# Optimization experiments

Hardware: AMD Instinct MI355X
Metric: run time of the kernel (lower is better)

Reference implementation:

```python
import jax, jax.numpy as jnp
import numpy as np

N = 50000     # nodes
E = 800000    # edges (avg degree 16)
IN, HID, OUT = 128, 128, 64


def setup_inputs() -> dict:
    key = jax.random.key(0)
    ks = jax.random.split(key, 12)
    x = jax.random.normal(ks[0], (N, IN), jnp.float32)
    src = jax.random.randint(ks[1], (E,), 0, N)
    dst = jax.random.randint(ks[2], (E,), 0, N)

    def lin(k, i, o):
        return (jax.random.normal(k, (i, o), jnp.float32) / np.sqrt(i)).astype(jnp.float32)

    return {
        "x": x, "src": src, "dst": dst,
        "Ws0": lin(ks[3], IN, HID), "Wn0": lin(ks[4], IN, HID), "b0": jnp.zeros((HID,), jnp.float32),
        "Ws1": lin(ks[5], HID, HID), "Wn1": lin(ks[6], HID, HID), "b1": jnp.zeros((HID,), jnp.float32),
        "Ws2": lin(ks[7], HID, OUT), "Wn2": lin(ks[8], HID, OUT), "b2": jnp.zeros((OUT,), jnp.float32),
    }


def reference(x, src, dst, Ws0, Wn0, b0, Ws1, Wn1, b1, Ws2, Wn2, b2):
    # in-degree for mean aggregation (clamped to 1 like DGL's mean reducer on non-empty mailboxes)
    deg = jnp.maximum(
        jax.ops.segment_sum(jnp.ones((E,), jnp.float32), dst, num_segments=N), 1.0
    )[:, None]

    def sage_conv(h, Ws, Wn, b):
        # gather src features, sum-reduce onto dst, divide by degree -> mean aggregation
        agg = jax.ops.segment_sum(h[src], dst, num_segments=N)  # [N, d]
        mean = agg / deg
        return h @ Ws + mean @ Wn + b

    h = jax.nn.relu(sage_conv(x, Ws0, Wn0, b0))   # dropout in eval mode -> identity
    h = jax.nn.relu(sage_conv(h, Ws1, Wn1, b1))
    return sage_conv(h, Ws2, Wn2, b2)
```

## Files before the change

kernel.cpp:

```cpp
#include <hip/hip_runtime.h>

#define CAP    64
#define PASSES 4
#define CSTRIDE 16

typedef __attribute__((ext_vector_type(8))) short bf16x8;
typedef __attribute__((ext_vector_type(4))) float f32x4;

__device__ __forceinline__ unsigned short f2bf(float f) {
    unsigned u = __builtin_bit_cast(unsigned, f);
    u += 0x7fffu + ((u >> 16) & 1u);
    return (unsigned short)(u >> 16);
}
__device__ __forceinline__ float bf2f(unsigned short h) {
    unsigned u = ((unsigned)h) << 16;
    return __builtin_bit_cast(float, u);
}

__device__ __forceinline__ void gload_lds16(const void* g, void* lds) {
    __builtin_amdgcn_global_load_lds(
        (const __attribute__((address_space(1))) void*)g,
        (__attribute__((address_space(3))) void*)lds, 16, 0, 0);
}

__global__ __launch_bounds__(256)
void fill_bucket_kernel(const int* __restrict__ src, const int* __restrict__ dst,
                        int* __restrict__ cnt, unsigned short* __restrict__ slot,
                        int E, int nPerPass) {
    int t  = blockIdx.x * 256 + threadIdx.x;
    int e0 = t * 4;
    if (e0 >= E) return;
    int4 s4, d4;
    if (e0 + 4 <= E) {
        s4 = *reinterpret_cast<const int4*>(src + e0);
        d4 = *reinterpret_cast<const int4*>(dst + e0);
    } else {
        int r = E - e0;
        s4.x = src[e0];                  d4.x = dst[e0];
        s4.y = (r > 1) ? src[e0 + 1] : 0; d4.y = (r > 1) ? dst[e0 + 1] : -1;
        s4.z = (r > 2) ? src[e0 + 2] : 0; d4.z = (r > 2) ? dst[e0 + 2] : -1;
        s4.w = 0;                         d4.w = -1;
    }
    #pragma unroll
    for (int p = 0; p < PASSES; p++) {
        const int lo = p * nPerPass, hi = lo + nPerPass;
        if (d4.x >= lo && d4.x < hi) {
            int q = atomicAdd(&cnt[(size_t)d4.x * CSTRIDE], 1);
            if (q < CAP) slot[(size_t)d4.x * CAP + q] = (unsigned short)s4.x;
        }
        if (d4.y >= lo && d4.y < hi) {
            int q = atomicAdd(&cnt[(size_t)d4.y * CSTRIDE], 1);
            if (q < CAP) slot[(size_t)d4.y * CAP + q] = (unsigned short)s4.y;
        }
        if (d4.z >= lo && d4.z < hi) {
            int q = atomicAdd(&cnt[(size_t)d4.z * CSTRIDE], 1);
            if (q < CAP) slot[(size_t)d4.z * CAP + q] = (unsigned short)s4.z;
        }
        if (d4.w >= lo && d4.w < hi) {
            int q = atomicAdd(&cnt[(size_t)d4.w * CSTRIDE], 1);
            if (q < CAP) slot[(size_t)d4.w * CAP + q] = (unsigned short)s4.w;
        }
    }
}

__global__ __launch_bounds__(256)
void split_x_kernel(const float* __restrict__ x, unsigned short* __restrict__ xhi,
                    unsigned short* __restrict__ xlo, long long total4)
{
    long long i = (long long)blockIdx.x * 256 + threadIdx.x;
    if (i >= total4) return;
    float4 v = reinterpret_cast<const float4*>(x)[i];
    float f[4] = {v.x, v.y, v.z, v.w};
    unsigned short h4[4], l4[4];
    #pragma unroll
    for (int j = 0; j < 4; j++) {
        h4[j] = f2bf(f[j]);
        l4[j] = f2bf(f[j] - bf2f(h4[j]));
    }
    reinterpret_cast<ushort4*>(xhi)[i] = make_ushort4(h4[0], h4[1], h4[2], h4[3]);
    reinterpret_cast<ushort4*>(xlo)[i] = make_ushort4(l4[0], l4[1], l4[2], l4[3]);
}

__global__ __launch_bounds__(256)
void prep_w_all_kernel(const float* __restrict__ Ws0, const float* __restrict__ Wn0,
                       const float* __restrict__ Ws1, const float* __restrict__ Wn1,
                       const float* __restrict__ Ws2, const float* __restrict__ Wn2,
                       unsigned short* __restrict__ Wh0, unsigned short* __restrict__ Wl0,
                       unsigned short* __restrict__ Wh1, unsigned short* __restrict__ Wl1,
                       unsigned short* __restrict__ Wh2, unsigned short* __restrict__ Wl2)
{
    int b = blockIdx.x;
    const float *Ws, *Wn;
    unsigned short *Wthi, *Wtlo;
    int D, idx;
    if (b < 128)      { Ws = Ws0; Wn = Wn0; Wthi = Wh0; Wtlo = Wl0; D = 128; idx = b * 256 + threadIdx.x; }
    else if (b < 256) { Ws = Ws1; Wn = Wn1; Wthi = Wh1; Wtlo = Wl1; D = 128; idx = (b - 128) * 256 + threadIdx.x; }
    else              { Ws = Ws2; Wn = Wn2; Wthi = Wh2; Wtlo = Wl2; D = 64;  idx = (b - 256) * 256 + threadIdx.x; }
    int DT = 2 * D;
    if (idx >= 128 * DT) return;
    int k = idx / DT, col = idx % DT;
    float v = (col < D) ? Ws[k * D + col] : Wn[k * D + (col - D)];
    unsigned short hi = f2bf(v);
    unsigned short lo = f2bf(v - bf2f(hi));
    Wthi[col * 128 + k] = hi;
    Wtlo[col * 128 + k] = lo;
}

template<int DTOT>
__global__ __launch_bounds__(256)
void mfma_dual_kernel(const unsigned short* __restrict__ hhi, const unsigned short* __restrict__ hlo,
                      const unsigned short* __restrict__ Wthi, const unsigned short* __restrict__ Wtlo,
                      const float* __restrict__ bias,
                      float* __restrict__ hs, unsigned short* __restrict__ hn, int N)
{
    constexpr int D  = DTOT / 2;
    constexpr int NT = DTOT / 64;
    constexpr int MT = 4;

    __shared__ unsigned short Ahi_l[64 * 128];
    __shared__ unsigned short Alo_l[64 * 128];

    const int tid = threadIdx.x;
    const int wv  = tid >> 6;
    const int l   = tid & 63;
    const int lm  = l & 15;
    const int kg  = l >> 4;
    const int block0  = blockIdx.x * 64;
    const int colbase = wv * (NT * 16);

    {
        const int row_l = (l >> 4);
        const int col16 = l & 15;
        #pragma unroll
        for (int i = 0; i < 4; i++) {
            const int ldsoff = wv * 4096 + i * 1024;
            int row = wv * 16 + i * 4 + row_l;
            int k2  = ((col16 ^ (row & 15)) << 4);
            int rg  = block0 + row; if (rg > N - 1) rg = N - 1;
            gload_lds16((const char*)hhi + (size_t)rg * 256 + k2, (char*)Ahi_l + ldsoff);
            gload_lds16((const char*)hlo + (size_t)rg * 256 + k2, (char*)Alo_l + ldsoff);
        }
    }
    asm volatile("s_waitcnt vmcnt(0)" ::: "memory");
    __syncthreads();

    f32x4 acc[MT][NT];
    #pragma unroll
    for (int mt = 0; mt < MT; mt++)
        #pragma unroll
        for (int nt = 0; nt < NT; nt++)
            acc[mt][nt] = (f32x4){0.f, 0.f, 0.f, 0.f};

    const size_t bofs = (size_t)(colbase + lm) * 128 + kg * 8;

    #pragma unroll
    for (int c = 0; c < 4; c++) {
        bf16x8 bh[NT], bl[NT];
        #pragma unroll
        for (int nt = 0; nt < NT; nt++) {
            const size_t bo = bofs + (size_t)nt * 16 * 128 + c * 32;
            bh[nt] = *reinterpret_cast<const bf16x8*>(Wthi + bo);
            bl[nt] = *reinterpret_cast<const bf16x8*>(Wtlo + bo);
        }
        bf16x8 ah[MT], al[MT];
        #pragma unroll
        for (int mt = 0; mt < MT; mt++) {
            const int r   = mt * 16 + lm;
            const int off = r * 128 + (((kg + 4 * c) ^ lm) << 3);
            ah[mt] = *reinterpret_cast<const bf16x8*>(&Ahi_l[off]);
            al[mt] = *reinterpret_cast<const bf16x8*>(&Alo_l[off]);
        }
        #pragma unroll
        for (int nt = 0; nt < NT; nt++)
            #pragma unroll
            for (int mt = 0; mt < MT; mt++) {
                acc[mt][nt] = __builtin_amdgcn_mfma_f32_16x16x32_bf16(ah[mt], bh[nt], acc[mt][nt], 0, 0, 0);
                acc[mt][nt] = __builtin_amdgcn_mfma_f32_16x16x32_bf16(ah[mt], bl[nt], acc[mt][nt], 0, 0, 0);
                acc[mt][nt] = __builtin_amdgcn_mfma_f32_16x16x32_bf16(al[mt], bh[nt], acc[mt][nt], 0, 0, 0);
            }
    }

    #pragma unroll
    for (int nt = 0; nt < NT; nt++) {
        const int col = colbase + nt * 16 + lm;
        const float bb = (col < D) ? bias[col] : 0.f;
        #pragma unroll
        for (int mt = 0; mt < MT; mt++) {
            #pragma unroll
            for (int i = 0; i < 4; i++) {
                int n = block0 + mt * 16 + kg * 4 + i;
                if (n >= N) continue;
                float v = acc[mt][nt][i];
                if (col < D) hs[(size_t)n * D + col] = v + bb;
                else         hn[(size_t)n * D + (col - D)] = f2bf(v);
            }
        }
    }
}

template<int D, bool RELU, bool SPLIT>
__global__ __launch_bounds__(256)
void gather_finish_kernel(const unsigned short* __restrict__ hn, const float* __restrict__ hs,
                          const int* __restrict__ cnt, const unsigned short* __restrict__ slot,
                          unsigned short* __restrict__ ohi, unsigned short* __restrict__ olo,
                          float* __restrict__ ofp, int N)
{
    const int node = (int)(((size_t)blockIdx.x * blockDim.x + threadIdx.x) >> 6);
    const int lane = threadIdx.x & 63;
    if (node >= N) return;

    int deg = cnt[(size_t)node * CSTRIDE];
    if (deg > CAP) deg = CAP;

    const int si = (int)slot[(size_t)node * CAP + lane];

    float p0 = 0.f, p1 = 0.f, q0 = 0.f, q1 = 0.f;
    float r0a = 0.f, r1a = 0.f, t0 = 0.f, t1 = 0.f;

    for (int j = 0; j < deg; j += 8) {
        unsigned u[8];
        bool ok[8];
        #pragma unroll
        for (int k = 0; k < 8; k++) {
            int jj = j + k;
            int s = __shfl(si, jj, 64);
            if (s > N - 1) s = N - 1;
            if (s < 0) s = 0;
            ok[k] = jj < deg;
            if constexpr (D == 128)
                u[k] = *reinterpret_cast<const unsigned*>(&hn[(size_t)s * D + lane * 2]);
            else
                u[k] = (unsigned)hn[(size_t)s * D + lane];
        }
        #pragma unroll
        for (int k = 0; k < 8; k++) {
            float f0 = ok[k] ? bf2f((unsigned short)(u[k] & 0xffffu)) : 0.f;
            if constexpr (D == 128) {
                float f1 = ok[k] ? bf2f((unsigned short)(u[k] >> 16)) : 0.f;
                switch (k & 3) {
                    case 0: p0 += f0; p1 += f1; break;
                    case 1: q0 += f0; q1 += f1; break;
                    case 2: r0a += f0; r1a += f1; break;
                    default: t0 += f0; t1 += f1; break;
                }
            } else {
                switch (k & 3) {
                    case 0: p0 += f0; break;
                    case 1: q0 += f0; break;
                    case 2: r0a += f0; break;
                    default: t0 += f0; break;
                }
            }
        }
    }
    float acc0 = (p0 + q0) + (r0a + t0);
    float acc1 = (p1 + q1) + (r1a + t1);

    const float inv = 1.0f / (float)(deg > 1 ? deg : 1);

    if constexpr (D == 128) {
        float2 s2 = *reinterpret_cast<const float2*>(&hs[(size_t)node * D + lane * 2]);
        float v0 = fmaf(acc0, inv, s2.x);
        float v1 = fmaf(acc1, inv, s2.y);
        if (RELU) { v0 = fmaxf(v0, 0.f); v1 = fmaxf(v1, 0.f); }
        if constexpr (SPLIT) {
            unsigned short h0 = f2bf(v0), h1 = f2bf(v1);
            unsigned short l0 = f2bf(v0 - bf2f(h0)), l1 = f2bf(v1 - bf2f(h1));
            *reinterpret_cast<unsigned*>(&ohi[(size_t)node * D + lane * 2]) = (unsigned)h0 | ((unsigned)h1 << 16);
            *reinterpret_cast<unsigned*>(&olo[(size_t)node * D + lane * 2]) = (unsigned)l0 | ((unsigned)l1 << 16);
        } else {
            *reinterpret_cast<float2*>(&ofp[(size_t)node * D + lane * 2]) = make_float2(v0, v1);
        }
    } else {
        float s1 = hs[(size_t)node * D + lane];
        float v = fmaf(acc0, inv, s1);
        if (RELU) v = fmaxf(v, 0.f);
        if constexpr (SPLIT) {
            unsigned short h0 = f2bf(v);
            ohi[(size_t)node * D + lane] = h0;
            olo[(size_t)node * D + lane] = f2bf(v - bf2f(h0));
        } else {
            ofp[(size_t)node * D + lane] = v;
        }
    }
}

extern "C" void kernel_launch(void* const* d_in, const int* in_sizes, int n_in,
                              void* d_out, int out_size, void* d_ws, size_t ws_size,
                              hipStream_t stream)
{
    const float* x   = (const float*)d_in[0];
    const int*   src = (const int*)d_in[1];
    const int*   dst = (const int*)d_in[2];
    const float* Ws0 = (const float*)d_in[3];
    const float* Wn0 = (const float*)d_in[4];
    const float* b0  = (const float*)d_in[5];
    const float* Ws1 = (const float*)d_in[6];
    const float* Wn1 = (const float*)d_in[7];
    const float* b1  = (const float*)d_in[8];
    const float* Ws2 = (const float*)d_in[9];
    const float* Wn2 = (const float*)d_in[10];
    const float* b2  = (const float*)d_in[11];
    float* out = (float*)d_out;

    const int N = in_sizes[0] / 128;
    const int E = in_sizes[1];

    char* ws = (char*)d_ws;
    size_t off = 0;
    auto alloc = [&](size_t bytes) -> void* {
        void* p = ws + off;
        off += (bytes + 255) & ~(size_t)255;
        return p;
    };
    int*            cnt   = (int*)           alloc((size_t)N * CSTRIDE * 4);
    unsigned short* slot  = (unsigned short*)alloc((size_t)N * CAP * 2);
    unsigned short* xhi   = (unsigned short*)alloc((size_t)N * 128 * 2);
    unsigned short* xlo   = (unsigned short*)alloc((size_t)N * 128 * 2);
    float*          hsb   = (float*)         alloc((size_t)N * 128 * 4);
    unsigned short* hnb   = (unsigned short*)alloc((size_t)N * 128 * 2);
    unsigned short* Wh0   = (unsigned short*)alloc(256 * 128 * 2);
    unsigned short* Wl0   = (unsigned short*)alloc(256 * 128 * 2);
    unsigned short* Wh1   = (unsigned short*)alloc(256 * 128 * 2);
    unsigned short* Wl1   = (unsigned short*)alloc(256 * 128 * 2);
    unsigned short* Wh2   = (unsigned short*)alloc(128 * 128 * 2);
    unsigned short* Wl2   = (unsigned short*)alloc(128 * 128 * 2);

    hipMemsetAsync(cnt, 0, (size_t)N * CSTRIDE * 4, stream);
    const int nPerPass = (N + PASSES - 1) / PASSES;
    fill_bucket_kernel<<<(E / 4 + 255) / 256, 256, 0, stream>>>(src, dst, cnt, slot, E, nPerPass);

    long long total4 = (long long)N * 32;
    split_x_kernel<<<(int)((total4 + 255) / 256), 256, 0, stream>>>(x, xhi, xlo, total4);
    prep_w_all_kernel<<<320, 256, 0, stream>>>(Ws0, Wn0, Ws1, Wn1, Ws2, Wn2,
                                               Wh0, Wl0, Wh1, Wl1, Wh2, Wl2);

    const int rowTiles = (N + 63) / 64;
    const int gblocks  = (N + 3) / 4;

    mfma_dual_kernel<256><<<rowTiles, 256, 0, stream>>>(xhi, xlo, Wh0, Wl0, b0, hsb, hnb, N);
    gather_finish_kernel<128, true, true><<<gblocks, 256, 0, stream>>>(hnb, hsb, cnt, slot, xhi, xlo, nullptr, N);

    mfma_dual_kernel<256><<<rowTiles, 256, 0, stream>>>(xhi, xlo, Wh1, Wl1, b1, hsb, hnb, N);
    gather_finish_kernel<128, true, true><<<gblocks, 256, 0, stream>>>(hnb, hsb, cnt, slot, xhi, xlo, nullptr, N);

    mfma_dual_kernel<128><<<rowTiles, 256, 0, stream>>>(xhi, xlo, Wh2, Wl2, b2, hsb, hnb, N);
    gather_finish_kernel<64, false, false><<<gblocks, 256, 0, stream>>>(hnb, hsb, cnt, slot, nullptr, nullptr, out, N);
}
```

Measured before the change: 244.5 us.

## Replicate per-node edge buckets across block groups and compact to dense adjacency

Replaces the 4-pass atomic bucket fill with one pass that spreads each node's counter and slots over 8 replicas chosen by block index, which reduces atomic contention on hot counters. A new compaction kernel prefix-sums the replica counts per node and writes a dense 64-entry slot list plus a degree array for the gather kernels. This adds a kernel launch and extra memory traffic. It also caps each replica at 16 entries, so skewed degrees could drop edges that the old single 64-slot bucket kept.

```diff
diff --git a/kernel.cpp b/kernel.cpp
--- a/kernel.cpp
+++ b/kernel.cpp
@@ -1,8 +1,8 @@
 #include <hip/hip_runtime.h>
 
-#define CAP    64
-#define PASSES 4
-#define CSTRIDE 16
+#define CAP   64
+#define NREP  8
+#define CAPR  16
 
 typedef __attribute__((ext_vector_type(8))) short bf16x8;
 typedef __attribute__((ext_vector_type(4))) float f32x4;
@@ -25,42 +25,70 @@
 
 __global__ __launch_bounds__(256)
 void fill_bucket_kernel(const int* __restrict__ src, const int* __restrict__ dst,
-                        int* __restrict__ cnt, unsigned short* __restrict__ slot,
-                        int E, int nPerPass) {
+                        int* __restrict__ cnt8, unsigned short* __restrict__ slot8, int E) {
     int t  = blockIdx.x * 256 + threadIdx.x;
     int e0 = t * 4;
     if (e0 >= E) return;
+    const int r = blockIdx.x & (NREP - 1);
     int4 s4, d4;
     if (e0 + 4 <= E) {
         s4 = *reinterpret_cast<const int4*>(src + e0);
         d4 = *reinterpret_cast<const int4*>(dst + e0);
     } else {
-        int r = E - e0;
-        s4.x = src[e0];                  d4.x = dst[e0];
-        s4.y = (r > 1) ? src[e0 + 1] : 0; d4.y = (r > 1) ? dst[e0 + 1] : -1;
-        s4.z = (r > 2) ? src[e0 + 2] : 0; d4.z = (r > 2) ? dst[e0 + 2] : -1;
-        s4.w = 0;                         d4.w = -1;
-    }
-    #pragma unroll
-    for (int p = 0; p < PASSES; p++) {
-        const int lo = p * nPerPass, hi = lo + nPerPass;
-        if (d4.x >= lo && d4.x < hi) {
-            int q = atomicAdd(&cnt[(size_t)d4.x * CSTRIDE], 1);
-            if (q < CAP) slot[(size_t)d4.x * CAP + q] = (unsigned short)s4.x;
-        }
-        if (d4.y >= lo && d4.y < hi) {
-            int q = atomicAdd(&cnt[(size_t)d4.y * CSTRIDE], 1);
-            if (q < CAP) slot[(size_t)d4.y * CAP + q] = (unsigned short)s4.y;
-        }
-        if (d4.z >= lo && d4.z < hi) {
-            int q = atomicAdd(&cnt[(size_t)d4.z * CSTRIDE], 1);
-            if (q < CAP) slot[(size_t)d4.z * CAP + q] = (unsigned short)s4.z;
-        }
-        if (d4.w >= lo && d4.w < hi) {
-            int q = atomicAdd(&cnt[(size_t)d4.w * CSTRIDE], 1);
-            if (q < CAP) slot[(size_t)d4.w * CAP + q] = (unsigned short)s4.w;
-        }
-    }
+        int rr = E - e0;
+        s4.x = src[e0];                   d4.x = dst[e0];
+        s4.y = (rr > 1) ? src[e0 + 1] : 0; d4.y = (rr > 1) ? dst[e0 + 1] : -1;
+        s4.z = (rr > 2) ? src[e0 + 2] : 0; d4.z = (rr > 2) ? dst[e0 + 2] : -1;
+        s4.w = 0;                          d4.w = -1;
+    }
+    if (d4.x >= 0) {
+        int q = atomicAdd(&cnt8[(size_t)d4.x * NREP + r], 1);
+        if (q < CAPR) slot8[(size_t)d4.x * (NREP * CAPR) + r * CAPR + q] = (unsigned short)s4.x;
+    }
+    if (d4.y >= 0) {
+        int q = atomicAdd(&cnt8[(size_t)d4.y * NREP + r], 1);
+        if (q < CAPR) slot8[(size_t)d4.y * (NREP * CAPR) + r * CAPR + q] = (unsigned short)s4.y;
+    }
+    if (d4.z >= 0) {
+        int q = atomicAdd(&cnt8[(size_t)d4.z * NREP + r], 1);
+        if (q < CAPR) slot8[(size_t)d4.z * (NREP * CAPR) + r * CAPR + q] = (unsigned short)s4.z;
+    }
+    if (d4.w >= 0) {
+        int q = atomicAdd(&cnt8[(size_t)d4.w * NREP + r], 1);
+        if (q < CAPR) slot8[(size_t)d4.w * (NREP * CAPR) + r * CAPR + q] = (unsigned short)s4.w;
+    }
+}
+
+__global__ __launch_bounds__(256)
+void compact_kernel(const int* __restrict__ cnt8, const unsigned short* __restrict__ slot8,
+                    unsigned short* __restrict__ dense, int* __restrict__ deg, int N) {
+    const int node = (int)(((size_t)blockIdx.x * blockDim.x + threadIdx.x) >> 6);
+    const int l    = threadIdx.x & 63;
+    if (node >= N) return;
+
+    int cr = 0;
+    if (l < NREP) {
+        cr = cnt8[(size_t)node * NREP + l];
+        if (cr > CAPR) cr = CAPR;
+    }
+    int pre = cr;
+    #pragma unroll
+    for (int o = 1; o < NREP; o <<= 1) {
+        int v = __shfl_up(pre, o, 64);
+        if (l >= o) pre += v;
+    }
+    const int myr = l >> 3;
+    const int c   = __shfl(cr, myr, 64);
+    const int b   = __shfl(pre - cr, myr, 64);
+    int tot = __shfl(pre, NREP - 1, 64);
+    if (tot > CAP) tot = CAP;
+
+    unsigned ent = *reinterpret_cast<const unsigned*>(slot8 + (size_t)node * (NREP * CAPR) + 2 * l);
+    const int q0 = 2 * (l & 7), q1 = q0 + 1;
+    const int p0 = b + q0,      p1 = b + q1;
+    if (q0 < c && p0 < CAP) dense[(size_t)node * CAP + p0] = (unsigned short)(ent & 0xffffu);
+    if (q1 < c && p1 < CAP) dense[(size_t)node * CAP + p1] = (unsigned short)(ent >> 16);
+    if (l == 0) deg[node] = tot;
 }
 
 __global__ __launch_bounds__(256)
@@ -201,7 +229,7 @@
 template<int D, bool RELU, bool SPLIT>
 __global__ __launch_bounds__(256)
 void gather_finish_kernel(const unsigned short* __restrict__ hn, const float* __restrict__ hs,
-                          const int* __restrict__ cnt, const unsigned short* __restrict__ slot,
+                          const int* __restrict__ deg_arr, const unsigned short* __restrict__ dense,
                           unsigned short* __restrict__ ohi, unsigned short* __restrict__ olo,
                           float* __restrict__ ofp, int N)
 {
@@ -209,10 +237,10 @@
     const int lane = threadIdx.x & 63;
     if (node >= N) return;
 
-    int deg = cnt[(size_t)node * CSTRIDE];
+    int deg = deg_arr[node];
     if (deg > CAP) deg = CAP;
 
-    const int si = (int)slot[(size_t)node * CAP + lane];
+    const int si = (int)dense[(size_t)node * CAP + lane];
 
     float p0 = 0.f, p1 = 0.f, q0 = 0.f, q1 = 0.f;
     float r0a = 0.f, r1a = 0.f, t0 = 0.f, t1 = 0.f;
@@ -313,8 +341,10 @@
         off += (bytes + 255) & ~(size_t)255;
         return p;
     };
-    int*            cnt   = (int*)           alloc((size_t)N * CSTRIDE * 4);
-    unsigned short* slot  = (unsigned short*)alloc((size_t)N * CAP * 2);
+    int*            cnt8  = (int*)           alloc((size_t)N * NREP * 4);
+    unsigned short* slot8 = (unsigned short*)alloc((size_t)N * NREP * CAPR * 2);
+    unsigned short* dense = (unsigned short*)alloc((size_t)N * CAP * 2);
+    int*            deg   = (int*)           alloc((size_t)N * 4);
     unsigned short* xhi   = (unsigned short*)alloc((size_t)N * 128 * 2);
     unsigned short* xlo   = (unsigned short*)alloc((size_t)N * 128 * 2);
     float*          hsb   = (float*)         alloc((size_t)N * 128 * 4);
@@ -326,9 +356,9 @@
     unsigned short* Wh2   = (unsigned short*)alloc(128 * 128 * 2);
     unsigned short* Wl2   = (unsigned short*)alloc(128 * 128 * 2);
 
-    hipMemsetAsync(cnt, 0, (size_t)N * CSTRIDE * 4, stream);
-    const int nPerPass = (N + PASSES - 1) / PASSES;
-    fill_bucket_kernel<<<(E / 4 + 255) / 256, 256, 0, stream>>>(src, dst, cnt, slot, E, nPerPass);
+    hipMemsetAsync(cnt8, 0, (size_t)N * NREP * 4, stream);
+    fill_bucket_kernel<<<(E / 4 + 255) / 256, 256, 0, stream>>>(src, dst, cnt8, slot8, E);
+    compact_kernel<<<(N + 3) / 4, 256, 0, stream>>>(cnt8, slot8, dense, deg, N);
 
     long long total4 = (long long)N * 32;
     split_x_kernel<<<(int)((total4 + 255) / 256), 256, 0, stream>>>(x, xhi, xlo, total4);
@@ -339,11 +369,11 @@
     const int gblocks  = (N + 3) / 4;
 
     mfma_dual_kernel<256><<<rowTiles, 256, 0, stream>>>(xhi, xlo, Wh0, Wl0, b0, hsb, hnb, N);
-    gather_finish_kernel<128, true, true><<<gblocks, 256, 0, stream>>>(hnb, hsb, cnt, slot, xhi, xlo, nullptr, N);
+    gather_finish_kernel<128, true, true><<<gblocks, 256, 0, stream>>>(hnb, hsb, deg, dense, xhi, xlo, nullptr, N);
 
     mfma_dual_kernel<256><<<rowTiles, 256, 0, stream>>>(xhi, xlo, Wh1, Wl1, b1, hsb, hnb, N);
-    gather_finish_kernel<128, true, true><<<gblocks, 256, 0, stream>>>(hnb, hsb, cnt, slot, xhi, xlo, nullptr, N);
+    gather_finish_kernel<128, true, true><<<gblocks, 256, 0, stream>>>(hnb, hsb, deg, dense, xhi, xlo, nullptr, N);
 
     mfma_dual_kernel<128><<<rowTiles, 256, 0, stream>>>(xhi, xlo, Wh2, Wl2, b2, hsb, hnb, N);
-    gather_finish_kernel<64, false, false><<<gblocks, 256, 0, stream>>>(hnb, hsb, cnt, slot, nullptr, nullptr, out, N);
-}
+    gather_finish_kernel<64, false, false><<<gblocks, 256, 0, stream>>>(hnb, hsb, deg, dense, nullptr, nullptr, out, N);
+}
```

After: 263.7 us. 7.8% more time.

## Merge x/W prep into one launch and co-run edge bucketing with layer-0 GEMM

Applied to the files above, without the earlier changes.

Combines the x split and weight prep kernels into a single launch. It also fuses the edge-bucket fill with the first-layer MFMA GEMM into one grid, with even blocks doing the GEMM and odd blocks doing the fill, so the atomic-heavy fill overlaps with compute. This removes two launches and their serialization gaps. The cost is that every fused block reserves GEMM shared memory, which may lower occupancy for the fill blocks.

```diff
diff --git a/kernel.cpp b/kernel.cpp
--- a/kernel.cpp
+++ b/kernel.cpp
@@ -1,7 +1,7 @@
 #include <hip/hip_runtime.h>
 
-#define CAP    64
-#define PASSES 4
+#define CAP     64
+#define PASSES  4
 #define CSTRIDE 16
 
 typedef __attribute__((ext_vector_type(8))) short bf16x8;
@@ -23,11 +23,11 @@
         (__attribute__((address_space(3))) void*)lds, 16, 0, 0);
 }
 
-__global__ __launch_bounds__(256)
-void fill_bucket_kernel(const int* __restrict__ src, const int* __restrict__ dst,
-                        int* __restrict__ cnt, unsigned short* __restrict__ slot,
-                        int E, int nPerPass) {
-    int t  = blockIdx.x * 256 + threadIdx.x;
+__device__ __forceinline__ void fill_body(int fb, int tid,
+                                          const int* __restrict__ src, const int* __restrict__ dst,
+                                          int* __restrict__ cnt, unsigned short* __restrict__ slot,
+                                          int E, int nPerPass) {
+    int t  = fb * 256 + tid;
     int e0 = t * 4;
     if (e0 >= E) return;
     int4 s4, d4;
@@ -36,7 +36,7 @@
         d4 = *reinterpret_cast<const int4*>(dst + e0);
     } else {
         int r = E - e0;
-        s4.x = src[e0];                  d4.x = dst[e0];
+        s4.x = src[e0];                   d4.x = dst[e0];
         s4.y = (r > 1) ? src[e0 + 1] : 0; d4.y = (r > 1) ? dst[e0 + 1] : -1;
         s4.z = (r > 2) ? src[e0 + 2] : 0; d4.z = (r > 2) ? dst[e0 + 2] : -1;
         s4.w = 0;                         d4.w = -1;
@@ -63,33 +63,154 @@
     }
 }
 
+template<int DTOT>
+__device__ __forceinline__ void mfma_body(int bx, int tid,
+        const unsigned short* __restrict__ hhi, const unsigned short* __restrict__ hlo,
+        const unsigned short* __restrict__ Wthi, const unsigned short* __restrict__ Wtlo,
+        const float* __restrict__ bias, float* __restrict__ hs, unsigned short* __restrict__ hn,
+        int N, unsigned short* Ahi_l, unsigned short* Alo_l)
+{
+    constexpr int D  = DTOT / 2;
+    constexpr int NT = DTOT / 64;
+    constexpr int MT = 4;
+    const int wv  = tid >> 6;
+    const int l   = tid & 63;
+    const int lm  = l & 15;
+    const int kg  = l >> 4;
+    const int block0  = bx * 64;
+    const int colbase = wv * (NT * 16);
+
+    {
+        const int row_l = (l >> 4);
+        const int col16 = l & 15;
+        #pragma unroll
+        for (int i = 0; i < 4; i++) {
+            const int ldsoff = wv * 4096 + i * 1024;
+            int row = wv * 16 + i * 4 + row_l;
+            int k2  = ((col16 ^ (row & 15)) << 4);
+            int rg  = block0 + row; if (rg > N - 1) rg = N - 1;
+            gload_lds16((const char*)hhi + (size_t)rg * 256 + k2, (char*)Ahi_l + ldsoff);
+            gload_lds16((const char*)hlo + (size_t)rg * 256 + k2, (char*)Alo_l + ldsoff);
+        }
+    }
+    asm volatile("s_waitcnt vmcnt(0)" ::: "memory");
+    __syncthreads();
+
+    f32x4 acc[MT][NT];
+    #pragma unroll
+    for (int mt = 0; mt < MT; mt++)
+        #pragma unroll
+        for (int nt = 0; nt < NT; nt++)
+            acc[mt][nt] = (f32x4){0.f, 0.f, 0.f, 0.f};
+
+    const size_t bofs = (size_t)(colbase + lm) * 128 + kg * 8;
+
+    #pragma unroll
+    for (int c = 0; c < 4; c++) {
+        bf16x8 bh[NT], bl[NT];
+        #pragma unroll
+        for (int nt = 0; nt < NT; nt++) {
+            const size_t bo = bofs + (size_t)nt * 16 * 128 + c * 32;
+            bh[nt] = *reinterpret_cast<const bf16x8*>(Wthi + bo);
+            bl[nt] = *reinterpret_cast<const bf16x8*>(Wtlo + bo);
+        }
+        bf16x8 ah[MT], al[MT];
+        #pragma unroll
+        for (int mt = 0; mt < MT; mt++) {
+            const int r   = mt * 16 + lm;
+            const int off = r * 128 + (((kg + 4 * c) ^ lm) << 3);
+            ah[mt] = *reinterpret_cast<const bf16x8*>(&Ahi_l[off]);
+            al[mt] = *reinterpret_cast<const bf16x8*>(&Alo_l[off]);
+        }
+        #pragma unroll
+        for (int nt = 0; nt < NT; nt++)
+            #pragma unroll
+            for (int mt = 0; mt < MT; mt++) {
+                acc[mt][nt] = __builtin_amdgcn_mfma_f32_16x16x32_bf16(ah[mt], bh[nt], acc[mt][nt], 0, 0, 0);
+                acc[mt][nt] = __builtin_amdgcn_mfma_f32_16x16x32_bf16(ah[mt], bl[nt], acc[mt][nt], 0, 0, 0);
+                acc[mt][nt] = __builtin_amdgcn_mfma_f32_16x16x32_bf16(al[mt], bh[nt], acc[mt][nt], 0, 0, 0);
+            }
+    }
+
+    #pragma unroll
+    for (int nt = 0; nt < NT; nt++) {
+        const int col = colbase + nt * 16 + lm;
+        const float bb = (col < D) ? bias[col] : 0.f;
+        #pragma unroll
+        for (int mt = 0; mt < MT; mt++) {
+            #pragma unroll
+            for (int i = 0; i < 4; i++) {
+                int n = block0 + mt * 16 + kg * 4 + i;
+                if (n >= N) continue;
+                float v = acc[mt][nt][i];
+                if (col < D) hs[(size_t)n * D + col] = v + bb;
+                else         hn[(size_t)n * D + (col - D)] = f2bf(v);
+            }
+        }
+    }
+}
+
 __global__ __launch_bounds__(256)
-void split_x_kernel(const float* __restrict__ x, unsigned short* __restrict__ xhi,
-                    unsigned short* __restrict__ xlo, long long total4)
-{
-    long long i = (long long)blockIdx.x * 256 + threadIdx.x;
-    if (i >= total4) return;
-    float4 v = reinterpret_cast<const float4*>(x)[i];
-    float f[4] = {v.x, v.y, v.z, v.w};
-    unsigned short h4[4], l4[4];
-    #pragma unroll
-    for (int j = 0; j < 4; j++) {
-        h4[j] = f2bf(f[j]);
-        l4[j] = f2bf(f[j] - bf2f(h4[j]));
-    }
-    reinterpret_cast<ushort4*>(xhi)[i] = make_ushort4(h4[0], h4[1], h4[2], h4[3]);
-    reinterpret_cast<ushort4*>(xlo)[i] = make_ushort4(l4[0], l4[1], l4[2], l4[3]);
-}
-
+void mm_fill_kernel(const unsigned short* __restrict__ hhi, const unsigned short* __restrict__ hlo,
+                    const unsigned short* __restrict__ Wthi, const unsigned short* __restrict__ Wtlo,
+                    const float* __restrict__ bias, float* __restrict__ hs, unsigned short* __restrict__ hn,
+                    int N, int nMM,
+                    const int* __restrict__ src, const int* __restrict__ dst,
+                    int* __restrict__ cnt, unsigned short* __restrict__ slot, int E, int nPerPass, int nFill)
+{
+    __shared__ unsigned short Ahi_l[64 * 128];
+    __shared__ unsigned short Alo_l[64 * 128];
+    const int b = blockIdx.x;
+    if ((b & 1) == 0) {
+        int mb = b >> 1;
+        if (mb < nMM)
+            mfma_body<256>(mb, threadIdx.x, hhi, hlo, Wthi, Wtlo, bias, hs, hn, N, Ahi_l, Alo_l);
+    } else {
+        int fb = b >> 1;
+        if (fb < nFill)
+            fill_body(fb, threadIdx.x, src, dst, cnt, slot, E, nPerPass);
+    }
+}
+
+template<int DTOT>
 __global__ __launch_bounds__(256)
-void prep_w_all_kernel(const float* __restrict__ Ws0, const float* __restrict__ Wn0,
-                       const float* __restrict__ Ws1, const float* __restrict__ Wn1,
-                       const float* __restrict__ Ws2, const float* __restrict__ Wn2,
-                       unsigned short* __restrict__ Wh0, unsigned short* __restrict__ Wl0,
-                       unsigned short* __restrict__ Wh1, unsigned short* __restrict__ Wl1,
-                       unsigned short* __restrict__ Wh2, unsigned short* __restrict__ Wl2)
+void mfma_dual_kernel(const unsigned short* __restrict__ hhi, const unsigned short* __restrict__ hlo,
+                      const unsigned short* __restrict__ Wthi, const unsigned short* __restrict__ Wtlo,
+                      const float* __restrict__ bias,
+                      float* __restrict__ hs, unsigned short* __restrict__ hn, int N)
+{
+    __shared__ unsigned short Ahi_l[64 * 128];
+    __shared__ unsigned short Alo_l[64 * 128];
+    mfma_body<DTOT>(blockIdx.x, threadIdx.x, hhi, hlo, Wthi, Wtlo, bias, hs, hn, N, Ahi_l, Alo_l);
+}
+
+__global__ __launch_bounds__(256)
+void prep_kernel(const float* __restrict__ x, unsigned short* __restrict__ xhi,
+                 unsigned short* __restrict__ xlo, long long total4, int splitBlocks,
+                 const float* __restrict__ Ws0, const float* __restrict__ Wn0,
+                 const float* __restrict__ Ws1, const float* __restrict__ Wn1,
+                 const float* __restrict__ Ws2, const float* __restrict__ Wn2,
+                 unsigned short* __restrict__ Wh0, unsigned short* __restrict__ Wl0,
+                 unsigned short* __restrict__ Wh1, unsigned short* __restrict__ Wl1,
+                 unsigned short* __restrict__ Wh2, unsigned short* __restrict__ Wl2)
 {
     int b = blockIdx.x;
+    if (b < splitBlocks) {
+        long long i = (long long)b * 256 + threadIdx.x;
+        if (i >= total4) return;
+        float4 v = reinterpret_cast<const float4*>(x)[i];
+        float f[4] = {v.x, v.y, v.z, v.w};
+        unsigned short h4[4], l4[4];
+        #pragma unroll
+        for (int j = 0; j < 4; j++) {
+            h4[j] = f2bf(f[j]);
+            l4[j] = f2bf(f[j] - bf2f(h4[j]));
+        }
+        reinterpret_cast<ushort4*>(xhi)[i] = make_ushort4(h4[0], h4[1], h4[2], h4[3]);
+        reinterpret_cast<ushort4*>(xlo)[i] = make_ushort4(l4[0], l4[1], l4[2], l4[3]);
+        return;
+    }
+    b -= splitBlocks;
     const float *Ws, *Wn;
     unsigned short *Wthi, *Wtlo;
     int D, idx;
@@ -104,98 +225,6 @@
     unsigned short lo = f2bf(v - bf2f(hi));
     Wthi[col * 128 + k] = hi;
     Wtlo[col * 128 + k] = lo;
-}
-
-template<int DTOT>
-__global__ __launch_bounds__(256)
-void mfma_dual_kernel(const unsigned short* __restrict__ hhi, const unsigned short* __restrict__ hlo,
-                      const unsigned short* __restrict__ Wthi, const unsigned short* __restrict__ Wtlo,
-                      const float* __restrict__ bias,
-                      float* __restrict__ hs, unsigned short* __restrict__ hn, int N)
-{
-    constexpr int D  = DTOT / 2;
-    constexpr int NT = DTOT / 64;
-    constexpr int MT = 4;
-
-    __shared__ unsigned short Ahi_l[64 * 128];
-    __shared__ unsigned short Alo_l[64 * 128];
-
-    const int tid = threadIdx.x;
-    const int wv  = tid >> 6;
-    const int l   = tid & 63;
-    const int lm  = l & 15;
-    const int kg  = l >> 4;
-    const int block0  = blockIdx.x * 64;
-    const int colbase = wv * (NT * 16);
-
-    {
-        const int row_l = (l >> 4);
-        const int col16 = l & 15;
-        #pragma unroll
-        for (int i = 0; i < 4; i++) {
-            const int ldsoff = wv * 4096 + i * 1024;
-            int row = wv * 16 + i * 4 + row_l;
-            int k2  = ((col16 ^ (row & 15)) << 4);
-            int rg  = block0 + row; if (rg > N - 1) rg = N - 1;
-            gload_lds16((const char*)hhi + (size_t)rg * 256 + k2, (char*)Ahi_l + ldsoff);
-            gload_lds16((const char*)hlo + (size_t)rg * 256 + k2, (char*)Alo_l + ldsoff);
-        }
-    }
-    asm volatile("s_waitcnt vmcnt(0)" ::: "memory");
-    __syncthreads();
-
-    f32x4 acc[MT][NT];
-    #pragma unroll
-    for (int mt = 0; mt < MT; mt++)
-        #pragma unroll
-        for (int nt = 0; nt < NT; nt++)
-            acc[mt][nt] = (f32x4){0.f, 0.f, 0.f, 0.f};
-
-    const size_t bofs = (size_t)(colbase + lm) * 128 + kg * 8;
-
-    #pragma unroll
-    for (int c = 0; c < 4; c++) {
-        bf16x8 bh[NT], bl[NT];
-        #pragma unroll
-        for (int nt = 0; nt < NT; nt++) {
-            const size_t bo = bofs + (size_t)nt * 16 * 128 + c * 32;
-            bh[nt] = *reinterpret_cast<const bf16x8*>(Wthi + bo);
-            bl[nt] = *reinterpret_cast<const bf16x8*>(Wtlo + bo);
-        }
-        bf16x8 ah[MT], al[MT];
-        #pragma unroll
-        for (int mt = 0; mt < MT; mt++) {
-            const int r   = mt * 16 + lm;
-            const int off = r * 128 + (((kg + 4 * c) ^ lm) << 3);
-            ah[mt] = *reinterpret_cast<const bf16x8*>(&Ahi_l[off]);
-            al[mt] = *reinterpret_cast<const bf16x8*>(&Alo_l[off]);
-        }
-        #pragma unroll
-        for (int nt = 0; nt < NT; nt++)
-            #pragma unroll
-            for (int mt = 0; mt < MT; mt++) {
-                acc[mt][nt] = __builtin_amdgcn_mfma_f32_16x16x32_bf16(ah[mt], bh[nt], acc[mt][nt], 0, 0, 0);
-                acc[mt][nt] = __builtin_amdgcn_mfma_f32_16x16x32_bf16(ah[mt], bl[nt], acc[mt][nt], 0, 0, 0);
-                acc[mt][nt] = __builtin_amdgcn_mfma_f32_16x16x32_bf16(al[mt], bh[nt], acc[mt][nt], 0, 0, 0);
-            }
-    }
-
-    #pragma unroll
-    for (int nt = 0; nt < NT; nt++) {
-        const int col = colbase + nt * 16 + lm;
-        const float bb = (col < D) ? bias[col] : 0.f;
-        #pragma unroll
-        for (int mt = 0; mt < MT; mt++) {
-            #pragma unroll
-            for (int i = 0; i < 4; i++) {
-                int n = block0 + mt * 16 + kg * 4 + i;
-                if (n >= N) continue;
-                float v = acc[mt][nt][i];
-                if (col < D) hs[(size_t)n * D + col] = v + bb;
-                else         hn[(size_t)n * D + (col - D)] = f2bf(v);
-            }
-        }
-    }
 }
 
 template<int D, bool RELU, bool SPLIT>
@@ -327,18 +356,24 @@
     unsigned short* Wl2   = (unsigned short*)alloc(128 * 128 * 2);
 
     hipMemsetAsync(cnt, 0, (size_t)N * CSTRIDE * 4, stream);
+
+    long long total4 = (long long)N * 32;
+    const int splitBlocks = (int)((total4 + 255) / 256);
+    prep_kernel<<<splitBlocks + 320, 256, 0, stream>>>(
+        x, xhi, xlo, total4, splitBlocks,
+        Ws0, Wn0, Ws1, Wn1, Ws2, Wn2, Wh0, Wl0, Wh1, Wl1, Wh2, Wl2);
+
+    const int rowTiles = (N + 63) / 64;
+    const int nFill    = (E / 4 + 255) / 256;
     const int nPerPass = (N + PASSES - 1) / PASSES;
-    fill_bucket_kernel<<<(E / 4 + 255) / 256, 256, 0, stream>>>(src, dst, cnt, slot, E, nPerPass);
-
-    long long total4 = (long long)N * 32;
-    split_x_kernel<<<(int)((total4 + 255) / 256), 256, 0, stream>>>(x, xhi, xlo, total4);
-    prep_w_all_kernel<<<320, 256, 0, stream>>>(Ws0, Wn0, Ws1, Wn1, Ws2, Wn2,
-                                               Wh0, Wl0, Wh1, Wl1, Wh2, Wl2);
-
-    const int rowTiles = (N + 63) / 64;
     const int gblocks  = (N + 3) / 4;
 
-    mfma_dual_kernel<256><<<rowTiles, 256, 0, stream>>>(xhi, xlo, Wh0, Wl0, b0, hsb, hnb, N);
+    {
+        int nPair = rowTiles > nFill ? rowTiles : nFill;
+        mm_fill_kernel<<<2 * nPair, 256, 0, stream>>>(
+            xhi, xlo, Wh0, Wl0, b0, hsb, hnb, N, rowTiles,
+            src, dst, cnt, slot, E, nPerPass, nFill);
+    }
     gather_finish_kernel<128, true, true><<<gblocks, 256, 0, stream>>>(hnb, hsb, cnt, slot, xhi, xlo, nullptr, N);
 
     mfma_dual_kernel<256><<<rowTiles, 256, 0, stream>>>(xhi, xlo, Wh1, Wl1, b1, hsb, hnb, N);
```

Result: faster. 217.8 us (-10.9%).
